# Kernel optimization log

Hardware: AMD Instinct MI355X
Metric: run time of the kernel (lower is better)

Reference implementation:

```python
import jax, jax.numpy as jnp
import numpy as np


def _resize1d(x, axis, out_size):
    """Bilinear resize along one axis, align_corners=False (PyTorch semantics,
    no antialias). x: any shape; interpolates along `axis` to out_size."""
    in_size = x.shape[axis]
    src = (jnp.arange(out_size, dtype=jnp.float32) + 0.5) * (in_size / out_size) - 0.5
    src = jnp.clip(src, 0.0, in_size - 1)
    i0 = jnp.floor(src).astype(jnp.int32)
    i1 = jnp.minimum(i0 + 1, in_size - 1)
    w = (src - i0.astype(jnp.float32))
    x0 = jnp.take(x, i0, axis=axis)
    x1 = jnp.take(x, i1, axis=axis)
    shape = [1] * x.ndim
    shape[axis] = out_size
    w = w.reshape(shape)
    return x0 * (1.0 - w) + x1 * w


def bilinear_resize(x, h_out, w_out):
    """x: (..., H, W) -> (..., h_out, w_out), bilinear align_corners=False."""
    x = _resize1d(x, x.ndim - 2, h_out)
    x = _resize1d(x, x.ndim - 1, w_out)
    return x


def _deform_corr_single(f1, f2, off):
    """f1, f2: (C, H, W); off: (2, H, W) with off[0]=dx, off[1]=dy.
    Bilinearly sample f2 at (x+dx, y+dy) with zero padding outside, then
    channel dot-product with f1 -> (H, W)."""
    C, H, W = f1.shape
    ys, xs = jnp.meshgrid(jnp.arange(H, dtype=jnp.float32),
                          jnp.arange(W, dtype=jnp.float32), indexing='ij')
    sx = xs + off[0]
    sy = ys + off[1]
    x0 = jnp.floor(sx)
    y0 = jnp.floor(sy)
    x1 = x0 + 1.0
    y1 = y0 + 1.0
    wx1 = sx - x0
    wy1 = sy - y0
    wx0 = 1.0 - wx1
    wy0 = 1.0 - wy1

    def corner(yc, xc, w):
        valid = (xc >= 0) & (xc <= W - 1) & (yc >= 0) & (yc <= H - 1)
        xi = jnp.clip(xc, 0, W - 1).astype(jnp.int32)
        yi = jnp.clip(yc, 0, H - 1).astype(jnp.int32)
        vals = f2[:, yi, xi]  # (C, H, W) gather
        return vals * (w * valid.astype(f2.dtype))[None, :, :]

    sampled = (corner(y0, x0, wy0 * wx0) + corner(y0, x1, wy0 * wx1)
               + corner(y1, x0, wy1 * wx0) + corner(y1, x1, wy1 * wx1))
    return jnp.sum(f1 * sampled, axis=0)  # (H, W)


_deform_corr = jax.vmap(_deform_corr_single)  # batched over B

SCALES = [0, 1, 2]


def setup_inputs() -> dict:
    key = jax.random.key(0)
    k1, k2, k3 = jax.random.split(key, 3)
    B, C, H, W = 4, 128, 256, 256
    feat1 = jax.random.normal(k1, (B, C, H, W), dtype=jnp.float32)
    feat2 = jax.random.normal(k2, (B, C, H, W), dtype=jnp.float32)
    # offsets in a few-pixel range, as typical for deformable flow offsets
    offsets = jax.random.normal(k3, (B, 2 * len(SCALES), H, W), dtype=jnp.float32) * 4.0
    return {"feat1": feat1, "feat2": feat2, "offsets": offsets}


def reference(feat1, feat2, offsets):
    B, C, H, W = feat1.shape
    corrs = []
    for i, scale in enumerate(SCALES):
        off = offsets[:, 2 * i:2 * i + 2]
        if scale > 0:
            hs, ws = H // (2 ** scale), W // (2 ** scale)
            f1 = bilinear_resize(feat1, hs, ws)
            f2 = bilinear_resize(feat2, hs, ws)
            off = bilinear_resize(off, hs, ws) / (2.0 ** scale)
        else:
            f1, f2 = feat1, feat2
        corr = _deform_corr(f1, f2, off)  # (B, hs, ws)
        if scale > 0:
            corr = bilinear_resize(corr, H, W)
        corrs.append(corr)
    return jnp.stack(corrs, axis=1)  # (B, S, H, W)
```

## Files before the change

### kernel.cpp

```cpp
#include <hip/hip_runtime.h>

#define HH 256
#define WW 256
#define NB 4
#define NC 128
#define HW (HH * WW)

__device__ __forceinline__ float blo(unsigned int u) { return __uint_as_float(u << 16); }
__device__ __forceinline__ float bhi(unsigned int u) { return __uint_as_float(u & 0xffff0000u); }
__device__ __forceinline__ unsigned int bf16_rne(float f) {
    unsigned int u = __float_as_uint(f);
    return (u + 0x7fffu + ((u >> 16) & 1u)) >> 16;
}
__device__ __forceinline__ unsigned int pack_bf16(float a, float b) {
    return bf16_rne(a) | (bf16_rne(b) << 16);
}
union U4 { uint4 v; unsigned int w[4]; };

__global__ __launch_bounds__(256) void prep7_kernel(
        const float* __restrict__ feat1, const float* __restrict__ feat2,
        unsigned int* __restrict__ s0f1, unsigned int* __restrict__ s0f2) {
    __shared__ float lds[128 * 128];

    int z = blockIdx.z;
    int b = z & 3;
    const float* src = (z < 4 ? feat1 : feat2) + (size_t)b * NC * HW;
    unsigned int* s0 = (z < 4 ? s0f1 : s0f2);

    int y  = blockIdx.y;
    int bx = blockIdx.x;
    int tid = threadIdx.x;
    int w = tid >> 6;
    int l = tid & 63;

    {
        int half = l >> 5;
        int cc = l & 31;
        const float* rowbase = src + (size_t)y * WW + bx * 128;
#pragma unroll
        for (int k = 0; k < 16; ++k) {
            int cp = w * 16 + k;
            int e = (cp >> 2) & 7;
            int ch = 2 * cp + half;
            const float* g = rowbase + (size_t)ch * HW + 4 * (cc ^ e);
            __builtin_amdgcn_global_load_lds(
                (const __attribute__((address_space(1))) void*)g,
                (__attribute__((address_space(3))) void*)&lds[cp * 256],
                16, 0, 0);
        }
    }
    __syncthreads();

    int c8 = l & 15;
    int pq = l >> 4;
    int e = c8 & 7;
#pragma unroll
    for (int it = 0; it < 8; ++it) {
        int p = w * 32 + it * 4 + pq;
        int col = 4 * (((p >> 2) ^ e)) + (p & 3);
        U4 u;
#pragma unroll
        for (int j = 0; j < 4; ++j) {
            float lo = lds[(8 * c8 + 2 * j) * 128 + col];
            float hi = lds[(8 * c8 + 2 * j + 1) * 128 + col];
            u.w[j] = pack_bf16(lo, hi);
        }
        size_t pix = ((size_t)(b * HH + y) * WW + bx * 128 + p);
        *(uint4*)(s0 + pix * 64 + c8 * 4) = u.v;
    }
}

template <int SC>
__global__ __launch_bounds__(256) void ds_hwc(
        const unsigned int* __restrict__ s0f1, const unsigned int* __restrict__ s0f2,
        unsigned int* __restrict__ df1, unsigned int* __restrict__ df2) {
    constexpr int S = (SC == 1) ? 128 : 64;
    int z = blockIdx.y;
    int b = z & 3;
    const unsigned int* s0 = (z < 4 ? s0f1 : s0f2) + ((size_t)b * HH * WW) * 64;
    unsigned int* d = (z < 4 ? df1 : df2) + ((size_t)b * S * S) * 64;

    int tid = blockIdx.x * 256 + threadIdx.x;
    int c8 = tid & 15;
    int p = tid >> 4;
    int yo = p / S, xo = p % S;
    int yi = (SC == 1) ? 2 * yo : 4 * yo + 1;
    int xi = (SC == 1) ? 2 * xo : 4 * xo + 1;

    const unsigned int* p00 = s0 + ((size_t)(yi * WW + xi)) * 64 + c8 * 4;
    U4 a, bb, c, dd, o;
    a.v  = *(const uint4*)p00;
    bb.v = *(const uint4*)(p00 + 64);
    c.v  = *(const uint4*)(p00 + WW * 64);
    dd.v = *(const uint4*)(p00 + WW * 64 + 64);
#pragma unroll
    for (int j = 0; j < 4; ++j) {
        float lo = blo(a.w[j]) + blo(bb.w[j]) + blo(c.w[j]) + blo(dd.w[j]);
        float hi = bhi(a.w[j]) + bhi(bb.w[j]) + bhi(c.w[j]) + bhi(dd.w[j]);
        o.w[j] = pack_bf16(0.25f * lo, 0.25f * hi);
    }
    *(uint4*)(d + (size_t)p * 64 + c8 * 4) = o.v;
}

template <int SCALE>
__global__ void corr_hwc(const unsigned int* __restrict__ f1,
                         const unsigned int* __restrict__ f2,
                         const float* __restrict__ offs,
                         float* __restrict__ out) {
    constexpr int S = (SCALE == 0) ? 256 : (SCALE == 1 ? 128 : 64);
    constexpr int LOGS = (SCALE == 0) ? 8 : (SCALE == 1 ? 7 : 6);
    int tid = threadIdx.x;
    int lane = tid & 15;
    int pix = blockIdx.x * 16 + (tid >> 4);
    int b = pix >> (2 * LOGS);
    int p = pix & (S * S - 1);
    int y = p >> LOGS;
    int x = p & (S - 1);

    const float* offx = offs + ((size_t)b * 6 + 2 * SCALE) * (HH * WW);
    const float* offy = offx + HH * WW;
    float dx, dy;
    if constexpr (SCALE == 0) {
        dx = offx[y * WW + x];
        dy = offy[y * WW + x];
    } else if constexpr (SCALE == 1) {
        const float* px = offx + (2 * y) * WW + 2 * x;
        const float* py = offy + (2 * y) * WW + 2 * x;
        dx = 0.125f * (px[0] + px[1] + px[WW] + px[WW + 1]);
        dy = 0.125f * (py[0] + py[1] + py[WW] + py[WW + 1]);
    } else {
        const float* px = offx + (4 * y + 1) * WW + 4 * x + 1;
        const float* py = offy + (4 * y + 1) * WW + 4 * x + 1;
        dx = 0.0625f * (px[0] + px[1] + px[WW] + px[WW + 1]);
        dy = 0.0625f * (py[0] + py[1] + py[WW] + py[WW + 1]);
    }

    float sx = (float)x + dx;
    float sy = (float)y + dy;
    float x0f = floorf(sx), y0f = floorf(sy);
    float wx1 = sx - x0f, wy1 = sy - y0f;
    float wx0 = 1.0f - wx1, wy0 = 1.0f - wy1;
    int x0 = (int)x0f, y0 = (int)y0f;
    int x1 = x0 + 1, y1 = y0 + 1;
    bool vx0 = (x0 >= 0) & (x0 < S);
    bool vx1 = (x1 >= 0) & (x1 < S);
    bool vy0 = (y0 >= 0) & (y0 < S);
    bool vy1 = (y1 >= 0) & (y1 < S);
    float w00 = wy0 * wx0 * (float)(vy0 & vx0);
    float w01 = wy0 * wx1 * (float)(vy0 & vx1);
    float w10 = wy1 * wx0 * (float)(vy1 & vx0);
    float w11 = wy1 * wx1 * (float)(vy1 & vx1);
    int cx0 = min(max(x0, 0), S - 1), cx1 = min(max(x1, 0), S - 1);
    int cy0 = min(max(y0, 0), S - 1), cy1 = min(max(y1, 0), S - 1);
    size_t pb = (size_t)b << (2 * LOGS);
    size_t i00 = pb + (cy0 << LOGS) + cx0, i01 = pb + (cy0 << LOGS) + cx1;
    size_t i10 = pb + (cy1 << LOGS) + cx0, i11 = pb + (cy1 << LOGS) + cx1;

    int lo = lane * 4;
    U4 a, c00, c01, c10, c11;
    a.v   = *(const uint4*)(f1 + ((size_t)pix << 6) + lo);
    c00.v = *(const uint4*)(f2 + (i00 << 6) + lo);
    c01.v = *(const uint4*)(f2 + (i01 << 6) + lo);
    c10.v = *(const uint4*)(f2 + (i10 << 6) + lo);
    c11.v = *(const uint4*)(f2 + (i11 << 6) + lo);

    float acc = 0.0f;
#pragma unroll
    for (int j = 0; j < 4; ++j) {
        float s_lo = w00 * blo(c00.w[j]) + w01 * blo(c01.w[j]) + w10 * blo(c10.w[j]) + w11 * blo(c11.w[j]);
        float s_hi = w00 * bhi(c00.w[j]) + w01 * bhi(c01.w[j]) + w10 * bhi(c10.w[j]) + w11 * bhi(c11.w[j]);
        acc = fmaf(blo(a.w[j]), s_lo, acc);
        acc = fmaf(bhi(a.w[j]), s_hi, acc);
    }
    acc += __shfl_xor(acc, 8);
    acc += __shfl_xor(acc, 4);
    acc += __shfl_xor(acc, 2);
    acc += __shfl_xor(acc, 1);

    if (lane == 0) {
        if constexpr (SCALE == 0) {
            out[((size_t)b * 3) * (HH * WW) + p] = acc;
        } else {
            out[(size_t)b * (S * S) + p] = acc;
        }
    }
}

template <int SCALE>
__global__ void up_kernel(const float* __restrict__ corr, float* __restrict__ out) {
    constexpr int S = (SCALE == 1) ? 128 : 64;
    constexpr float R = (float)S / 256.0f;
    int idx = blockIdx.x * blockDim.x + threadIdx.x;
    if (idx >= NB * HH * WW) return;
    int x = idx & 255;
    int t = idx >> 8;
    int y = t & 255;
    int b = t >> 8;
    float srcx = fminf(fmaxf(((float)x + 0.5f) * R - 0.5f, 0.0f), (float)(S - 1));
    float srcy = fminf(fmaxf(((float)y + 0.5f) * R - 0.5f, 0.0f), (float)(S - 1));
    int x0 = (int)srcx;
    int y0 = (int)srcy;
    int x1 = min(x0 + 1, S - 1), y1 = min(y0 + 1, S - 1);
    float wx = srcx - (float)x0, wy = srcy - (float)y0;
    const float* cp = corr + (size_t)b * (S * S);
    float v0 = cp[y0 * S + x0] * (1.0f - wx) + cp[y0 * S + x1] * wx;
    float v1 = cp[y1 * S + x0] * (1.0f - wx) + cp[y1 * S + x1] * wx;
    out[((size_t)b * 3 + SCALE) * (HH * WW) + y * WW + x] = (1.0f - wy) * v0 + wy * v1;
}

extern "C" void kernel_launch(void* const* d_in, const int* in_sizes, int n_in,
                              void* d_out, int out_size, void* d_ws, size_t ws_size,
                              hipStream_t stream) {
    const float* feat1 = (const float*)d_in[0];
    const float* feat2 = (const float*)d_in[1];
    const float* offs  = (const float*)d_in[2];
    float* out = (float*)d_out;

    const size_t n_s0 = (size_t)NB * HH * WW * 64;
    const size_t n_d1 = (size_t)NB * 128 * 128 * 64;
    const size_t n_d2 = (size_t)NB * 64 * 64 * 64;
    const size_t n_c1 = (size_t)NB * 128 * 128;
    const size_t n_c2 = (size_t)NB * 64 * 64;
    const size_t need = (2 * (n_s0 + n_d1 + n_d2) + n_c1 + n_c2) * 4;
    if (ws_size < need) return;

    unsigned int* ws = (unsigned int*)d_ws;
    unsigned int* s0f1 = ws;
    unsigned int* s0f2 = s0f1 + n_s0;
    unsigned int* d1f1 = s0f2 + n_s0;
    unsigned int* d1f2 = d1f1 + n_d1;
    unsigned int* d2f1 = d1f2 + n_d1;
    unsigned int* d2f2 = d2f1 + n_d2;
    float* corr1 = (float*)(d2f2 + n_d2);
    float* corr2 = corr1 + n_c1;

    prep7_kernel<<<dim3(2, 256, 8), 256, 0, stream>>>(feat1, feat2, s0f1, s0f2);

    ds_hwc<1><<<dim3(1024, 8), 256, 0, stream>>>(s0f1, s0f2, d1f1, d1f2);
    ds_hwc<2><<<dim3(256, 8), 256, 0, stream>>>(s0f1, s0f2, d2f1, d2f2);

    corr_hwc<0><<<NB * 65536 / 16, 256, 0, stream>>>(s0f1, s0f2, offs, out);
    corr_hwc<1><<<NB * 16384 / 16, 256, 0, stream>>>(d1f1, d1f2, offs, corr1);
    corr_hwc<2><<<NB * 4096 / 16, 256, 0, stream>>>(d2f1, d2f2, offs, corr2);

    up_kernel<1><<<(NB * HH * WW + 255) / 256, 256, 0, stream>>>(corr1, out);
    up_kernel<2><<<(NB * HH * WW + 255) / 256, 256, 0, stream>>>(corr2, out);
}
```

Before: 143.6 us.

## Fuse half-resolution downsample into the CHW-to-HWC bf16 prep kernel

The prep kernel now converts fp32 to bf16 before staging in LDS, and each block processes a pair of image rows for a 32-channel group. That pair is exactly the 2x2 footprint needed for the half-resolution level, so the block writes both the full-resolution HWC bf16 tensor and the scale-1 downsampled tensor. This removes the separate ds_hwc<1> launch and its re-read of the scale-0 buffer. In exchange it drops the async global_load_lds path, halves LDS use, and averages bf16-rounded values rather than the fp32 inputs, which changes rounding slightly.

```diff
diff --git a/kernel.cpp b/kernel.cpp
--- a/kernel.cpp
+++ b/kernel.cpp
@@ -17,56 +17,74 @@
 }
 union U4 { uint4 v; unsigned int w[4]; };
 
-__global__ __launch_bounds__(256) void prep7_kernel(
+__global__ __launch_bounds__(256) void prep8_kernel(
         const float* __restrict__ feat1, const float* __restrict__ feat2,
-        unsigned int* __restrict__ s0f1, unsigned int* __restrict__ s0f2) {
-    __shared__ float lds[128 * 128];
-
-    int z = blockIdx.z;
+        unsigned int* __restrict__ s0f1, unsigned int* __restrict__ s0f2,
+        unsigned int* __restrict__ d1f1, unsigned int* __restrict__ d1f2) {
+    __shared__ unsigned int lds[32 * 258];
+
+    int z = blockIdx.y;
     int b = z & 3;
     const float* src = (z < 4 ? feat1 : feat2) + (size_t)b * NC * HW;
     unsigned int* s0 = (z < 4 ? s0f1 : s0f2);
-
-    int y  = blockIdx.y;
-    int bx = blockIdx.x;
+    unsigned int* d1 = (z < 4 ? d1f1 : d1f2);
+
+    int cg = blockIdx.x & 3;
+    int y2 = blockIdx.x >> 2;
     int tid = threadIdx.x;
-    int w = tid >> 6;
-    int l = tid & 63;
-
-    {
-        int half = l >> 5;
-        int cc = l & 31;
-        const float* rowbase = src + (size_t)y * WW + bx * 128;
-#pragma unroll
-        for (int k = 0; k < 16; ++k) {
-            int cp = w * 16 + k;
-            int e = (cp >> 2) & 7;
-            int ch = 2 * cp + half;
-            const float* g = rowbase + (size_t)ch * HW + 4 * (cc ^ e);
-            __builtin_amdgcn_global_load_lds(
-                (const __attribute__((address_space(1))) void*)g,
-                (__attribute__((address_space(3))) void*)&lds[cp * 256],
-                16, 0, 0);
+
+    const float* base = src + (size_t)(32 * cg) * HW + y2 * 512;
+#pragma unroll
+    for (int i = 0; i < 16; ++i) {
+        int f4 = i * 256 + tid;
+        int ch = f4 >> 7;
+        int pos = f4 & 127;
+        float4 v = *(const float4*)(base + (size_t)ch * HW + 4 * pos);
+        unsigned int w0 = pack_bf16(v.x, v.y);
+        unsigned int w1 = pack_bf16(v.z, v.w);
+        *(uint2*)&lds[ch * 258 + 2 * pos] = make_uint2(w0, w1);
+    }
+    __syncthreads();
+
+#pragma unroll
+    for (int it = 0; it < 8; ++it) {
+        int item = it * 256 + tid;
+        int q = item & 3;
+        int p = item >> 2;
+        int pp = p >> 1, h = p & 1;
+        U4 o;
+#pragma unroll
+        for (int j = 0; j < 4; ++j) {
+            int u = 4 * q + j;
+            unsigned int wA = lds[(2 * u) * 258 + pp];
+            unsigned int wB = lds[(2 * u + 1) * 258 + pp];
+            o.w[j] = h ? ((wA >> 16) | (wB & 0xffff0000u))
+                       : ((wA & 0xffffu) | (wB << 16));
         }
-    }
-    __syncthreads();
-
-    int c8 = l & 15;
-    int pq = l >> 4;
-    int e = c8 & 7;
-#pragma unroll
-    for (int it = 0; it < 8; ++it) {
-        int p = w * 32 + it * 4 + pq;
-        int col = 4 * (((p >> 2) ^ e)) + (p & 3);
-        U4 u;
+        int r = p >> 8, x = p & 255;
+        size_t pix = ((size_t)(b * HH + 2 * y2 + r) * WW + x);
+        *(uint4*)(s0 + pix * 64 + 16 * cg + 4 * q) = o.v;
+    }
+
+#pragma unroll
+    for (int it = 0; it < 2; ++it) {
+        int item = it * 256 + tid;
+        int q = item & 3;
+        int xq = item >> 2;
+        U4 o;
 #pragma unroll
         for (int j = 0; j < 4; ++j) {
-            float lo = lds[(8 * c8 + 2 * j) * 128 + col];
-            float hi = lds[(8 * c8 + 2 * j + 1) * 128 + col];
-            u.w[j] = pack_bf16(lo, hi);
+            int u = 4 * q + j;
+            unsigned int a0 = lds[(2 * u) * 258 + xq];
+            unsigned int a1 = lds[(2 * u) * 258 + 128 + xq];
+            unsigned int b0 = lds[(2 * u + 1) * 258 + xq];
+            unsigned int b1 = lds[(2 * u + 1) * 258 + 128 + xq];
+            float avA = 0.25f * (blo(a0) + bhi(a0) + blo(a1) + bhi(a1));
+            float avB = 0.25f * (blo(b0) + bhi(b0) + blo(b1) + bhi(b1));
+            o.w[j] = pack_bf16(avA, avB);
         }
-        size_t pix = ((size_t)(b * HH + y) * WW + bx * 128 + p);
-        *(uint4*)(s0 + pix * 64 + c8 * 4) = u.v;
+        size_t pix = ((size_t)(b * 128 + y2) * 128 + xq);
+        *(uint4*)(d1 + pix * 64 + 16 * cg + 4 * q) = o.v;
     }
 }
 
@@ -234,9 +252,9 @@
     float* corr1 = (float*)(d2f2 + n_d2);
     float* corr2 = corr1 + n_c1;
 
-    prep7_kernel<<<dim3(2, 256, 8), 256, 0, stream>>>(feat1, feat2, s0f1, s0f2);
-
-    ds_hwc<1><<<dim3(1024, 8), 256, 0, stream>>>(s0f1, s0f2, d1f1, d1f2);
+    prep8_kernel<<<dim3(512, 8), 256, 0, stream>>>(feat1, feat2, s0f1, s0f2,
+                                                   d1f1, d1f2);
+
     ds_hwc<2><<<dim3(256, 8), 256, 0, stream>>>(s0f1, s0f2, d2f1, d2f2);
 
     corr_hwc<0><<<NB * 65536 / 16, 256, 0, stream>>>(s0f1, s0f2, offs, out);
```

Result: faster. 139.5 us (-2.9%).

## Fuse scale-1 downsample into the transpose/bf16 prep kernel

Applied to the files above, without the earlier changes.

The prep kernel now handles two input rows per block, converts each to the bf16 HWC layout as before, and accumulates 2x2 fp32 averages in registers to write the scale-1 downsampled features directly. This removes the separate ds_hwc<1> launch and its re-read of the s0 buffer. It also averages from fp32 rather than bf16-rounded values. The cost is more registers, an extra barrier per phase, and half as many blocks in the grid.

```diff
diff --git a/kernel.cpp b/kernel.cpp
--- a/kernel.cpp
+++ b/kernel.cpp
@@ -17,56 +17,88 @@
 }
 union U4 { uint4 v; unsigned int w[4]; };
 
-__global__ __launch_bounds__(256) void prep7_kernel(
+__global__ __launch_bounds__(256) void prep9_kernel(
         const float* __restrict__ feat1, const float* __restrict__ feat2,
-        unsigned int* __restrict__ s0f1, unsigned int* __restrict__ s0f2) {
+        unsigned int* __restrict__ s0f1, unsigned int* __restrict__ s0f2,
+        unsigned int* __restrict__ d1f1, unsigned int* __restrict__ d1f2) {
     __shared__ float lds[128 * 128];
 
     int z = blockIdx.z;
     int b = z & 3;
     const float* src = (z < 4 ? feat1 : feat2) + (size_t)b * NC * HW;
     unsigned int* s0 = (z < 4 ? s0f1 : s0f2);
-
-    int y  = blockIdx.y;
+    unsigned int* d1 = (z < 4 ? d1f1 : d1f2);
+
+    int y2 = blockIdx.y;
     int bx = blockIdx.x;
     int tid = threadIdx.x;
     int w = tid >> 6;
     int l = tid & 63;
 
-    {
-        int half = l >> 5;
-        int cc = l & 31;
-        const float* rowbase = src + (size_t)y * WW + bx * 128;
-#pragma unroll
-        for (int k = 0; k < 16; ++k) {
-            int cp = w * 16 + k;
-            int e = (cp >> 2) & 7;
-            int ch = 2 * cp + half;
-            const float* g = rowbase + (size_t)ch * HW + 4 * (cc ^ e);
-            __builtin_amdgcn_global_load_lds(
-                (const __attribute__((address_space(1))) void*)g,
-                (__attribute__((address_space(3))) void*)&lds[cp * 256],
-                16, 0, 0);
+    int half = l >> 5;
+    int cc = l & 31;
+    int c8 = l & 15;
+    int pr = l >> 4;
+    int e = c8 & 7;
+
+    float accLo[4][4], accHi[4][4];
+#pragma unroll
+    for (int i = 0; i < 4; ++i)
+#pragma unroll
+        for (int j = 0; j < 4; ++j) { accLo[i][j] = 0.0f; accHi[i][j] = 0.0f; }
+
+#pragma unroll
+    for (int phase = 0; phase < 2; ++phase) {
+        int row = 2 * y2 + phase;
+        {
+            const float* rowbase = src + (size_t)row * WW + bx * 128;
+#pragma unroll
+            for (int k = 0; k < 16; ++k) {
+                int cp = w * 16 + k;
+                int ed = (cp >> 2) & 7;
+                int ch = 2 * cp + half;
+                const float* g = rowbase + (size_t)ch * HW + 4 * (cc ^ ed);
+                __builtin_amdgcn_global_load_lds(
+                    (const __attribute__((address_space(1))) void*)g,
+                    (__attribute__((address_space(3))) void*)&lds[cp * 256],
+                    16, 0, 0);
+            }
         }
-    }
-    __syncthreads();
-
-    int c8 = l & 15;
-    int pq = l >> 4;
-    int e = c8 & 7;
-#pragma unroll
-    for (int it = 0; it < 8; ++it) {
-        int p = w * 32 + it * 4 + pq;
-        int col = 4 * (((p >> 2) ^ e)) + (p & 3);
-        U4 u;
-#pragma unroll
-        for (int j = 0; j < 4; ++j) {
-            float lo = lds[(8 * c8 + 2 * j) * 128 + col];
-            float hi = lds[(8 * c8 + 2 * j + 1) * 128 + col];
-            u.w[j] = pack_bf16(lo, hi);
+        __syncthreads();
+
+        size_t rowpix = ((size_t)(b * HH + row) * WW + bx * 128);
+#pragma unroll
+        for (int it = 0; it < 4; ++it) {
+            int m = it * 16 + w * 4 + pr;
+            int col0 = 4 * ((m >> 1) ^ e) + 2 * (m & 1);
+            U4 u0, u1;
+#pragma unroll
+            for (int j = 0; j < 4; ++j) {
+                int ch = 8 * c8 + 2 * j;
+                float lo0 = lds[ch * 128 + col0];
+                float lo1 = lds[ch * 128 + col0 + 1];
+                float hi0 = lds[(ch + 1) * 128 + col0];
+                float hi1 = lds[(ch + 1) * 128 + col0 + 1];
+                u0.w[j] = pack_bf16(lo0, hi0);
+                u1.w[j] = pack_bf16(lo1, hi1);
+                accLo[it][j] += lo0 + lo1;
+                accHi[it][j] += hi0 + hi1;
+            }
+            *(uint4*)(s0 + (rowpix + 2 * m) * 64 + c8 * 4) = u0.v;
+            *(uint4*)(s0 + (rowpix + 2 * m + 1) * 64 + c8 * 4) = u1.v;
         }
-        size_t pix = ((size_t)(b * HH + y) * WW + bx * 128 + p);
-        *(uint4*)(s0 + pix * 64 + c8 * 4) = u.v;
+        __syncthreads();
+    }
+
+    size_t d1row = ((size_t)(b * 128 + y2) * 128 + bx * 64);
+#pragma unroll
+    for (int it = 0; it < 4; ++it) {
+        int m = it * 16 + w * 4 + pr;
+        U4 o;
+#pragma unroll
+        for (int j = 0; j < 4; ++j)
+            o.w[j] = pack_bf16(0.25f * accLo[it][j], 0.25f * accHi[it][j]);
+        *(uint4*)(d1 + (d1row + m) * 64 + c8 * 4) = o.v;
     }
 }
 
@@ -234,9 +266,9 @@
     float* corr1 = (float*)(d2f2 + n_d2);
     float* corr2 = corr1 + n_c1;
 
-    prep7_kernel<<<dim3(2, 256, 8), 256, 0, stream>>>(feat1, feat2, s0f1, s0f2);
-
-    ds_hwc<1><<<dim3(1024, 8), 256, 0, stream>>>(s0f1, s0f2, d1f1, d1f2);
+    prep9_kernel<<<dim3(2, 128, 8), 256, 0, stream>>>(feat1, feat2, s0f1, s0f2,
+                                                      d1f1, d1f2);
+
     ds_hwc<2><<<dim3(256, 8), 256, 0, stream>>>(s0f1, s0f2, d2f1, d2f2);
 
     corr_hwc<0><<<NB * 65536 / 16, 256, 0, stream>>>(s0f1, s0f2, offs, out);
```

After: 130.3 us (median of 2 runs). -9.3%, faster.
